# Performance work log

Hardware: AMD Instinct MI355X
Metric: run time of the kernel (lower is better)

The kernel has to match this reference:

```python
import jax, jax.numpy as jnp
import numpy as np

B, S, D = 2, 2048, 1024
N_HEADS = 16
HEAD_DIM = D // N_HEADS  # 64, even for RoPE
THETA = 10000.0


def rope_tables(seq, head_dim, dtype=jnp.float32):
    half = head_dim // 2
    freqs = 1.0 / (THETA ** (jnp.arange(half, dtype=jnp.float32) / half))
    angles = jnp.arange(seq, dtype=jnp.float32)[:, None] * freqs[None, :]  # [S, half]
    return jnp.cos(angles).astype(dtype), jnp.sin(angles).astype(dtype)


def apply_rope_interleaved(x, cos, sin):
    # x: [b, h, s, d]; even/odd interleaving
    x_even = x[..., 0::2]
    x_odd = x[..., 1::2]
    r_even = x_even * cos - x_odd * sin
    r_odd = x_even * sin + x_odd * cos
    # interleave back: stack on last axis then reshape
    out = jnp.stack([r_even, r_odd], axis=-1).reshape(x.shape)
    return out


def setup_inputs() -> dict:
    key = jax.random.key(0)
    ks = jax.random.split(key, 6)
    scale = 1.0 / np.sqrt(D)
    return {
        "x": jax.random.normal(ks[0], (B, S, D), dtype=jnp.float32),
        "Wq": jax.random.normal(ks[1], (D, D), dtype=jnp.float32) * scale,
        "Wk": jax.random.normal(ks[2], (D, D), dtype=jnp.float32) * scale,
        "Wv": jax.random.normal(ks[3], (D, D), dtype=jnp.float32) * scale,
        "Wo": jax.random.normal(ks[4], (D, D), dtype=jnp.float32) * scale,
        "bo": jnp.zeros((D,), dtype=jnp.float32),
    }


def reference(x, Wq, Wk, Wv, Wo, bo):
    b, s, _ = x.shape
    # QKV projections (no bias), split heads -> [b, h, s, hd]
    def proj(W):
        return jnp.einsum('bsd,de->bse', x, W).reshape(b, s, N_HEADS, HEAD_DIM).transpose(0, 2, 1, 3)
    q, k, v = proj(Wq), proj(Wk), proj(Wv)

    cos, sin = rope_tables(s, HEAD_DIM, x.dtype)  # [s, hd//2]
    q = apply_rope_interleaved(q, cos, sin)
    k = apply_rope_interleaved(k, cos, sin)

    scale = 1.0 / jnp.sqrt(jnp.asarray(HEAD_DIM, dtype=x.dtype))
    scores = jnp.einsum('bhqd,bhkd->bhqk', q, k) * scale  # [b, h, s, s]
    causal = jnp.tril(jnp.ones((s, s), dtype=bool))
    scores = jnp.where(causal[None, None], scores, jnp.asarray(-jnp.inf, dtype=scores.dtype))
    attn = jax.nn.softmax(scores, axis=-1)
    ctx = jnp.einsum('bhqk,bhkd->bhqd', attn, v)  # [b, h, s, hd]
    ctx = ctx.transpose(0, 2, 1, 3).reshape(b, s, N_HEADS * HEAD_DIM)
    return jnp.einsum('bsd,de->bse', ctx, Wo) + bo
```

## Files before the change

### kernel.cpp

```cpp
#include <hip/hip_runtime.h>
#include <hip/hip_bf16.h>
#include <math.h>

constexpr int Bb   = 2;
constexpr int S    = 2048;
constexpr int D    = 1024;
constexpr int H    = 16;
constexpr int Dh   = 64;
constexpr int HALF = 32;
constexpr int M    = Bb * S;
constexpr int K    = 1024;
constexpr int N    = 1024;

typedef __attribute__((ext_vector_type(8))) short short8;
typedef __attribute__((ext_vector_type(4))) float f32x4;

__device__ __forceinline__ unsigned short f2bf(float f) {
    unsigned int u = __float_as_uint(f);
    unsigned int r = (u + 0x7fffu + ((u >> 16) & 1u)) >> 16;
    return (unsigned short)r;
}

__device__ __forceinline__ void gl_lds16(const unsigned short* g, unsigned short* lds_base) {
    __builtin_amdgcn_global_load_lds(
        (const __attribute__((address_space(1))) unsigned int*)g,
        (__attribute__((address_space(3))) unsigned int*)lds_base, 16, 0, 0);
}

__global__ void rope_table_kernel(float* __restrict__ cosT, float* __restrict__ sinT) {
    int idx = blockIdx.x * blockDim.x + threadIdx.x;
    if (idx >= S * HALF) return;
    int s = idx / HALF;
    int i = idx % HALF;
    double freq = exp(-(double)i * (log(10000.0) / (double)HALF));
    double ang  = (double)s * freq;
    cosT[idx] = (float)cos(ang);
    sinT[idx] = (float)sin(ang);
}

__global__ __launch_bounds__(256) void convx_kernel(const float* __restrict__ x,
                                                    unsigned short* __restrict__ xb) {
    size_t i = (size_t)blockIdx.x * 256 + threadIdx.x;
    float4 v = *(const float4*)(x + i * 4);
    ushort4 pk;
    pk.x = f2bf(v.x); pk.y = f2bf(v.y); pk.z = f2bf(v.z); pk.w = f2bf(v.w);
    *(ushort4*)(xb + i * 4) = pk;
}

__global__ __launch_bounds__(256) void wt_kernel(
    const float* W0, const float* W1, const float* W2, const float* W3,
    unsigned short* T0, unsigned short* T1, unsigned short* T2, unsigned short* T3)
{
    __shared__ float tile[64][65];
    int z = blockIdx.z;
    const float* W = (z == 0) ? W0 : (z == 1) ? W1 : (z == 2) ? W2 : W3;
    unsigned short* T = (z == 0) ? T0 : (z == 1) ? T1 : (z == 2) ? T2 : T3;

    const int bk = blockIdx.y * 64;
    const int bn = blockIdx.x * 64;
    const int tid = threadIdx.x;
    const int lr = tid >> 4;
    const int lc = (tid & 15) * 4;

    #pragma unroll
    for (int i = 0; i < 4; ++i) {
        int r = lr + i * 16;
        float4 v = *(const float4*)(W + (size_t)(bk + r) * N + bn + lc);
        tile[r][lc + 0] = v.x; tile[r][lc + 1] = v.y;
        tile[r][lc + 2] = v.z; tile[r][lc + 3] = v.w;
    }
    __syncthreads();
    #pragma unroll
    for (int i = 0; i < 4; ++i) {
        int nr = lr + i * 16;
        ushort4 pk;
        pk.x = f2bf(tile[lc + 0][nr]);
        pk.y = f2bf(tile[lc + 1][nr]);
        pk.z = f2bf(tile[lc + 2][nr]);
        pk.w = f2bf(tile[lc + 3][nr]);
        *(ushort4*)(T + (size_t)(bn + nr) * K + bk + lc) = pk;
    }
}

__global__ __launch_bounds__(256) void mfma_gemm_kernel(
    const unsigned short* __restrict__ A,
    const unsigned short* BTa, const unsigned short* BTb, const unsigned short* BTc,
    void* outa, void* outb, void* outc,
    const float* __restrict__ bias,
    const float* __restrict__ cosT, const float* __restrict__ sinT,
    int fused)
{
    __shared__ __align__(16) unsigned short As[128 * 32];
    __shared__ __align__(16) unsigned short Bs[128 * 32];

    const int z = blockIdx.z;
    const unsigned short* BT = (z == 0) ? BTa : (z == 1) ? BTb : BTc;
    void* outp = (z == 0) ? outa : (z == 1) ? outb : outc;
    const int mode = fused ? ((z == 2) ? 2 : 1) : 0;

    const int tid  = threadIdx.x;
    const int wave = tid >> 6;
    const int lane = tid & 63;
    const int col  = lane & 15;
    const int quad = lane >> 4;
    const int wy   = wave >> 1;
    const int wx   = wave & 1;

    const int mbase = blockIdx.y * 128;
    const int nbase = blockIdx.x * 128;

    const int srow   = lane >> 2;
    const int schunk = lane & 3;

    f32x4 acc[4][4];
    #pragma unroll
    for (int mi = 0; mi < 4; ++mi)
        #pragma unroll
        for (int ni = 0; ni < 4; ++ni) acc[mi][ni] = (f32x4)0.f;

    for (int k0 = 0; k0 < K; k0 += 32) {
        __syncthreads();
        #pragma unroll
        for (int L = 0; L < 2; ++L) {
            int wrow = L * 64 + wave * 16;
            int tr   = wrow + srow;
            int gc   = (schunk + tr) & 3;
            gl_lds16(A  + (size_t)(mbase + tr) * K + k0 + gc * 8, &As[wrow * 32]);
            gl_lds16(BT + (size_t)(nbase + tr) * K + k0 + gc * 8, &Bs[wrow * 32]);
        }
        __syncthreads();

        short8 af[4], bf[4];
        #pragma unroll
        for (int mi = 0; mi < 4; ++mi) {
            int r = wy * 64 + mi * 16 + col;
            af[mi] = *(const short8*)&As[r * 32 + ((quad - r) & 3) * 8];
        }
        #pragma unroll
        for (int ni = 0; ni < 4; ++ni) {
            int r = wx * 64 + ni * 16 + col;
            bf[ni] = *(const short8*)&Bs[r * 32 + ((quad - r) & 3) * 8];
        }
        #pragma unroll
        for (int mi = 0; mi < 4; ++mi)
            #pragma unroll
            for (int ni = 0; ni < 4; ++ni)
                acc[mi][ni] = __builtin_amdgcn_mfma_f32_16x16x32_bf16(af[mi], bf[ni], acc[mi][ni], 0, 0, 0);
    }

    if (mode == 0) {
        float* o = (float*)outp;
        #pragma unroll
        for (int ni = 0; ni < 4; ++ni) {
            int n_g = nbase + wx * 64 + ni * 16 + col;
            float bv = bias[n_g];
            #pragma unroll
            for (int mi = 0; mi < 4; ++mi)
                #pragma unroll
                for (int reg = 0; reg < 4; ++reg) {
                    int m_g = mbase + wy * 64 + mi * 16 + quad * 4 + reg;
                    o[(size_t)m_g * N + n_g] = acc[mi][ni][reg] + bv;
                }
        }
    } else if (mode == 1) {
        unsigned short* o = (unsigned short*)outp;
        #pragma unroll
        for (int ni = 0; ni < 4; ++ni) {
            int n_g = nbase + wx * 64 + ni * 16 + col;
            int h = n_g >> 6, dh0 = n_g & 63, p = dh0 >> 1;
            bool even = !(dh0 & 1);
            #pragma unroll
            for (int mi = 0; mi < 4; ++mi)
                #pragma unroll
                for (int reg = 0; reg < 4; ++reg) {
                    int m_g = mbase + wy * 64 + mi * 16 + quad * 4 + reg;
                    int b = m_g >> 11, s = m_g & 2047;
                    float v = acc[mi][ni][reg];
                    float part = __shfl_xor(v, 1, 64);
                    float c = cosT[s * HALF + p], sn = sinT[s * HALF + p];
                    float r = even ? (v * c - part * sn) : (v * c + part * sn);
                    o[((size_t)(b * H + h) * S + s) * Dh + dh0] = f2bf(r);
                }
        }
    } else {
        unsigned short* o = (unsigned short*)outp;
        #pragma unroll
        for (int ni = 0; ni < 4; ++ni) {
            int n_g = nbase + wx * 64 + ni * 16 + col;
            int h = n_g >> 6, dh0 = n_g & 63;
            #pragma unroll
            for (int mi = 0; mi < 4; ++mi) {
                int m0g = mbase + wy * 64 + mi * 16 + quad * 4;
                int b = m0g >> 11, s = m0g & 2047;
                ushort4 pk;
                pk.x = f2bf(acc[mi][ni][0]);
                pk.y = f2bf(acc[mi][ni][1]);
                pk.z = f2bf(acc[mi][ni][2]);
                pk.w = f2bf(acc[mi][ni][3]);
                *(ushort4*)&o[((size_t)(b * H + h) * Dh + dh0) * S + s] = pk;
            }
        }
    }
}

__global__ __launch_bounds__(256) void attn_mfma_kernel(
    const unsigned short* __restrict__ q, const unsigned short* __restrict__ k,
    const unsigned short* __restrict__ vt, unsigned short* __restrict__ ctx)
{
    __shared__ __align__(16) short Ks[64 * 64];
    __shared__ __align__(16) short Vs[64 * 64];
    __shared__ __align__(16) short Ps[4][16 * 72];

    const int tid  = threadIdx.x;
    const int wave = tid >> 6;
    const int lane = tid & 63;
    const int col  = lane & 15;
    const int quad = lane >> 4;
    const int l8   = lane >> 3, cp = lane & 7;

    const int bh = blockIdx.y;
    const unsigned short* qb = q  + (size_t)bh * S * Dh;
    const unsigned short* kb = k  + (size_t)bh * S * Dh;
    const unsigned short* vb = vt + (size_t)bh * Dh * S;
    const int b = bh >> 4, h = bh & 15;

    for (int phase = 0; phase < 2; ++phase) {
        const int qt  = phase ? (31 - (int)blockIdx.x) : (int)blockIdx.x;
        const int wr0 = qt * 64 + wave * 16;

        short8 qfrag[2];
        #pragma unroll
        for (int ks = 0; ks < 2; ++ks)
            qfrag[ks] = *(const short8*)(qb + (size_t)(wr0 + col) * Dh + ks * 32 + quad * 8);

        f32x4 O[4];
        float lacc[4];
        #pragma unroll
        for (int nt = 0; nt < 4; ++nt) O[nt] = (f32x4)0.f;
        #pragma unroll
        for (int r = 0; r < 4; ++r) lacc[r] = 0.f;

        short8 kr[2], vr[2];
        #pragma unroll
        for (int c = 0; c < 2; ++c) {
            int row = wave * 16 + c * 8 + l8;
            int sc  = (cp + row) & 7;
            kr[c] = *(const short8*)(kb + (size_t)row * Dh + sc * 8);
            vr[c] = *(const short8*)(vb + (size_t)row * S + sc * 8);
        }

        for (int t = 0; t <= qt; ++t) {
            __syncthreads();
            #pragma unroll
            for (int c = 0; c < 2; ++c) {
                int row = wave * 16 + c * 8 + l8;
                *(short8*)&Ks[row * 64 + cp * 8] = kr[c];
                *(short8*)&Vs[row * 64 + cp * 8] = vr[c];
            }
            __syncthreads();
            if (t < qt) {
                #pragma unroll
                for (int c = 0; c < 2; ++c) {
                    int row = wave * 16 + c * 8 + l8;
                    int sc  = (cp + row) & 7;
                    kr[c] = *(const short8*)(kb + (size_t)((t + 1) * 64 + row) * Dh + sc * 8);
                    vr[c] = *(const short8*)(vb + (size_t)row * S + (t + 1) * 64 + sc * 8);
                }
            }

            f32x4 sacc[4];
            #pragma unroll
            for (int nt = 0; nt < 4; ++nt) sacc[nt] = (f32x4)0.f;
            #pragma unroll
            for (int ks = 0; ks < 2; ++ks) {
                #pragma unroll
                for (int nt = 0; nt < 4; ++nt) {
                    int key = nt * 16 + col;
                    short8 kf = *(const short8*)&Ks[key * 64 + (((ks * 4 + quad) - key) & 7) * 8];
                    sacc[nt] = __builtin_amdgcn_mfma_f32_16x16x32_bf16(qfrag[ks], kf, sacc[nt], 0, 0, 0);
                }
            }

            float pb[4][4];
            #pragma unroll
            for (int nt = 0; nt < 4; ++nt) {
                int key_l = nt * 16 + col;
                #pragma unroll
                for (int reg = 0; reg < 4; ++reg) {
                    float e = __expf(fmaf(sacc[nt][reg], 0.125f, -8.0f));
                    if (t == qt && key_l > wave * 16 + quad * 4 + reg) e = 0.f;
                    pb[nt][reg] = e;
                }
            }
            #pragma unroll
            for (int reg = 0; reg < 4; ++reg)
                lacc[reg] += (pb[0][reg] + pb[1][reg]) + (pb[2][reg] + pb[3][reg]);

            #pragma unroll
            for (int nt = 0; nt < 4; ++nt)
                #pragma unroll
                for (int reg = 0; reg < 4; ++reg)
                    Ps[wave][(quad * 4 + reg) * 72 + nt * 16 + col] = (short)f2bf(pb[nt][reg]);

            #pragma unroll
            for (int ks = 0; ks < 2; ++ks) {
                short8 pf = *(const short8*)&Ps[wave][col * 72 + ks * 32 + quad * 8];
                #pragma unroll
                for (int nt = 0; nt < 4; ++nt) {
                    int dh = nt * 16 + col;
                    short8 vf = *(const short8*)&Vs[dh * 64 + (((ks * 4 + quad) - dh) & 7) * 8];
                    O[nt] = __builtin_amdgcn_mfma_f32_16x16x32_bf16(pf, vf, O[nt], 0, 0, 0);
                }
            }
        }

        #pragma unroll
        for (int reg = 0; reg < 4; ++reg) {
            float s = lacc[reg];
            #pragma unroll
            for (int off = 1; off <= 8; off <<= 1)
                s += __shfl_xor(s, off, 64);
            lacc[reg] = s;
        }

        #pragma unroll
        for (int reg = 0; reg < 4; ++reg) {
            float inv = 1.0f / lacc[reg];
            int rg = wr0 + quad * 4 + reg;
            unsigned short* dst = ctx + ((size_t)b * S + rg) * 1024 + h * 64 + col;
            #pragma unroll
            for (int nt = 0; nt < 4; ++nt)
                dst[nt * 16] = f2bf(O[nt][reg] * inv);
        }
    }
}

extern "C" void kernel_launch(void* const* d_in, const int* in_sizes, int n_in,
                              void* d_out, int out_size, void* d_ws, size_t ws_size,
                              hipStream_t stream) {
    const float* x  = (const float*)d_in[0];
    const float* Wq = (const float*)d_in[1];
    const float* Wk = (const float*)d_in[2];
    const float* Wv = (const float*)d_in[3];
    const float* Wo = (const float*)d_in[4];
    const float* bo = (const float*)d_in[5];
    float* out = (float*)d_out;

    const size_t MK  = (size_t)M * K;
    const size_t NK  = (size_t)N * K;
    const size_t QKV = (size_t)Bb * H * S * Dh;

    unsigned short* xb   = (unsigned short*)d_ws;
    unsigned short* WqT  = xb  + MK;
    unsigned short* WkT  = WqT + NK;
    unsigned short* WvT  = WkT + NK;
    unsigned short* WoT  = WvT + NK;
    unsigned short* qbuf = WoT + NK;
    unsigned short* kbuf = qbuf + QKV;
    unsigned short* vtb  = kbuf + QKV;
    unsigned short* ctxb = vtb  + QKV;
    float* cosT = (float*)(ctxb + QKV);
    float* sinT = cosT + (size_t)S * HALF;

    rope_table_kernel<<<(S * HALF + 255) / 256, 256, 0, stream>>>(cosT, sinT);
    convx_kernel<<<(int)(MK / 4 / 256), 256, 0, stream>>>(x, xb);
    wt_kernel<<<dim3(16, 16, 4), 256, 0, stream>>>(Wq, Wk, Wv, Wo, WqT, WkT, WvT, WoT);

    mfma_gemm_kernel<<<dim3(8, 32, 3), 256, 0, stream>>>(
        xb, WqT, WkT, WvT, qbuf, kbuf, vtb, nullptr, cosT, sinT, 1);

    attn_mfma_kernel<<<dim3(16, Bb * H), 256, 0, stream>>>(qbuf, kbuf, vtb, ctxb);

    mfma_gemm_kernel<<<dim3(8, 32, 1), 256, 0, stream>>>(
        ctxb, WoT, nullptr, nullptr, out, nullptr, nullptr, bo, cosT, sinT, 0);
}
```

Measured before the change: 211.1 us.

## Share A tile across fused Q/K/V projections with narrower N tiles

After: 222.8 us. +5.5%, slower.

```diff
diff --git a/kernel.cpp b/kernel.cpp
--- a/kernel.cpp
+++ b/kernel.cpp
@@ -82,21 +82,19 @@
     }
 }
 
+template<int NZ, int MODEQ>
 __global__ __launch_bounds__(256) void mfma_gemm_kernel(
     const unsigned short* __restrict__ A,
-    const unsigned short* BTa, const unsigned short* BTb, const unsigned short* BTc,
-    void* outa, void* outb, void* outc,
+    const unsigned short* BT0, const unsigned short* BT1, const unsigned short* BT2,
+    void* out0, void* out1, void* out2,
     const float* __restrict__ bias,
-    const float* __restrict__ cosT, const float* __restrict__ sinT,
-    int fused)
+    const float* __restrict__ cosT, const float* __restrict__ sinT)
 {
     __shared__ __align__(16) unsigned short As[128 * 32];
-    __shared__ __align__(16) unsigned short Bs[128 * 32];
-
-    const int z = blockIdx.z;
-    const unsigned short* BT = (z == 0) ? BTa : (z == 1) ? BTb : BTc;
-    void* outp = (z == 0) ? outa : (z == 1) ? outb : outc;
-    const int mode = fused ? ((z == 2) ? 2 : 1) : 0;
+    __shared__ __align__(16) unsigned short Bs[NZ][64 * 32];
+
+    const unsigned short* BT[3] = {BT0, BT1, BT2};
+    void* outs[3] = {out0, out1, out2};
 
     const int tid  = threadIdx.x;
     const int wave = tid >> 6;
@@ -107,16 +105,18 @@
     const int wx   = wave & 1;
 
     const int mbase = blockIdx.y * 128;
-    const int nbase = blockIdx.x * 128;
+    const int nbase = blockIdx.x * 64;
 
     const int srow   = lane >> 2;
     const int schunk = lane & 3;
 
-    f32x4 acc[4][4];
+    f32x4 acc[NZ][4][2];
     #pragma unroll
-    for (int mi = 0; mi < 4; ++mi)
-        #pragma unroll
-        for (int ni = 0; ni < 4; ++ni) acc[mi][ni] = (f32x4)0.f;
+    for (int z = 0; z < NZ; ++z)
+        #pragma unroll
+        for (int mi = 0; mi < 4; ++mi)
+            #pragma unroll
+            for (int ni = 0; ni < 2; ++ni) acc[z][mi][ni] = (f32x4)0.f;
 
     for (int k0 = 0; k0 < K; k0 += 32) {
         __syncthreads();
@@ -124,80 +124,95 @@
         for (int L = 0; L < 2; ++L) {
             int wrow = L * 64 + wave * 16;
             int tr   = wrow + srow;
-            int gc   = (schunk + tr) & 3;
-            gl_lds16(A  + (size_t)(mbase + tr) * K + k0 + gc * 8, &As[wrow * 32]);
-            gl_lds16(BT + (size_t)(nbase + tr) * K + k0 + gc * 8, &Bs[wrow * 32]);
+            int gc   = (schunk + (tr >> 1)) & 3;
+            gl_lds16(A + (size_t)(mbase + tr) * K + k0 + gc * 8, &As[wrow * 32]);
+        }
+        {
+            int wrow = wave * 16;
+            int tr   = wrow + srow;
+            int gc   = (schunk + (tr >> 1)) & 3;
+            #pragma unroll
+            for (int z = 0; z < NZ; ++z)
+                gl_lds16(BT[z] + (size_t)(nbase + tr) * K + k0 + gc * 8, &Bs[z][wrow * 32]);
         }
         __syncthreads();
 
-        short8 af[4], bf[4];
+        short8 af[4], bf[NZ][2];
         #pragma unroll
         for (int mi = 0; mi < 4; ++mi) {
             int r = wy * 64 + mi * 16 + col;
-            af[mi] = *(const short8*)&As[r * 32 + ((quad - r) & 3) * 8];
-        }
-        #pragma unroll
-        for (int ni = 0; ni < 4; ++ni) {
-            int r = wx * 64 + ni * 16 + col;
-            bf[ni] = *(const short8*)&Bs[r * 32 + ((quad - r) & 3) * 8];
-        }
-        #pragma unroll
-        for (int mi = 0; mi < 4; ++mi)
-            #pragma unroll
-            for (int ni = 0; ni < 4; ++ni)
-                acc[mi][ni] = __builtin_amdgcn_mfma_f32_16x16x32_bf16(af[mi], bf[ni], acc[mi][ni], 0, 0, 0);
-    }
-
-    if (mode == 0) {
-        float* o = (float*)outp;
-        #pragma unroll
-        for (int ni = 0; ni < 4; ++ni) {
-            int n_g = nbase + wx * 64 + ni * 16 + col;
-            float bv = bias[n_g];
+            af[mi] = *(const short8*)&As[r * 32 + ((quad - (r >> 1)) & 3) * 8];
+        }
+        #pragma unroll
+        for (int z = 0; z < NZ; ++z)
+            #pragma unroll
+            for (int ni = 0; ni < 2; ++ni) {
+                int r = wx * 32 + ni * 16 + col;
+                bf[z][ni] = *(const short8*)&Bs[z][r * 32 + ((quad - (r >> 1)) & 3) * 8];
+            }
+        #pragma unroll
+        for (int z = 0; z < NZ; ++z)
             #pragma unroll
             for (int mi = 0; mi < 4; ++mi)
                 #pragma unroll
-                for (int reg = 0; reg < 4; ++reg) {
-                    int m_g = mbase + wy * 64 + mi * 16 + quad * 4 + reg;
-                    o[(size_t)m_g * N + n_g] = acc[mi][ni][reg] + bv;
-                }
-        }
-    } else if (mode == 1) {
-        unsigned short* o = (unsigned short*)outp;
-        #pragma unroll
-        for (int ni = 0; ni < 4; ++ni) {
-            int n_g = nbase + wx * 64 + ni * 16 + col;
-            int h = n_g >> 6, dh0 = n_g & 63, p = dh0 >> 1;
-            bool even = !(dh0 & 1);
-            #pragma unroll
-            for (int mi = 0; mi < 4; ++mi)
-                #pragma unroll
-                for (int reg = 0; reg < 4; ++reg) {
-                    int m_g = mbase + wy * 64 + mi * 16 + quad * 4 + reg;
-                    int b = m_g >> 11, s = m_g & 2047;
-                    float v = acc[mi][ni][reg];
-                    float part = __shfl_xor(v, 1, 64);
-                    float c = cosT[s * HALF + p], sn = sinT[s * HALF + p];
-                    float r = even ? (v * c - part * sn) : (v * c + part * sn);
-                    o[((size_t)(b * H + h) * S + s) * Dh + dh0] = f2bf(r);
-                }
-        }
-    } else {
-        unsigned short* o = (unsigned short*)outp;
-        #pragma unroll
-        for (int ni = 0; ni < 4; ++ni) {
-            int n_g = nbase + wx * 64 + ni * 16 + col;
-            int h = n_g >> 6, dh0 = n_g & 63;
-            #pragma unroll
-            for (int mi = 0; mi < 4; ++mi) {
-                int m0g = mbase + wy * 64 + mi * 16 + quad * 4;
-                int b = m0g >> 11, s = m0g & 2047;
-                ushort4 pk;
-                pk.x = f2bf(acc[mi][ni][0]);
-                pk.y = f2bf(acc[mi][ni][1]);
-                pk.z = f2bf(acc[mi][ni][2]);
-                pk.w = f2bf(acc[mi][ni][3]);
-                *(ushort4*)&o[((size_t)(b * H + h) * Dh + dh0) * S + s] = pk;
+                for (int ni = 0; ni < 2; ++ni)
+                    acc[z][mi][ni] = __builtin_amdgcn_mfma_f32_16x16x32_bf16(
+                        af[mi], bf[z][ni], acc[z][mi][ni], 0, 0, 0);
+    }
+
+    #pragma unroll
+    for (int z = 0; z < NZ; ++z) {
+        if (MODEQ == 0) {
+            float* o = (float*)outs[z];
+            #pragma unroll
+            for (int ni = 0; ni < 2; ++ni) {
+                int n_g = nbase + wx * 32 + ni * 16 + col;
+                float bv = bias[n_g];
+                #pragma unroll
+                for (int mi = 0; mi < 4; ++mi)
+                    #pragma unroll
+                    for (int reg = 0; reg < 4; ++reg) {
+                        int m_g = mbase + wy * 64 + mi * 16 + quad * 4 + reg;
+                        o[(size_t)m_g * N + n_g] = acc[z][mi][ni][reg] + bv;
+                    }
+            }
+        } else if (z < 2) {
+            unsigned short* o = (unsigned short*)outs[z];
+            #pragma unroll
+            for (int ni = 0; ni < 2; ++ni) {
+                int n_g = nbase + wx * 32 + ni * 16 + col;
+                int h = n_g >> 6, dh0 = n_g & 63, p = dh0 >> 1;
+                bool even = !(dh0 & 1);
+                #pragma unroll
+                for (int mi = 0; mi < 4; ++mi)
+                    #pragma unroll
+                    for (int reg = 0; reg < 4; ++reg) {
+                        int m_g = mbase + wy * 64 + mi * 16 + quad * 4 + reg;
+                        int b = m_g >> 11, s = m_g & 2047;
+                        float v = acc[z][mi][ni][reg];
+                        float part = __shfl_xor(v, 1, 64);
+                        float c = cosT[s * HALF + p], sn = sinT[s * HALF + p];
+                        float r = even ? (v * c - part * sn) : (v * c + part * sn);
+                        o[((size_t)(b * H + h) * S + s) * Dh + dh0] = f2bf(r);
+                    }
+            }
+        } else {
+            unsigned short* o = (unsigned short*)outs[z];
+            #pragma unroll
+            for (int ni = 0; ni < 2; ++ni) {
+                int n_g = nbase + wx * 32 + ni * 16 + col;
+                int h = n_g >> 6, dh0 = n_g & 63;
+                #pragma unroll
+                for (int mi = 0; mi < 4; ++mi) {
+                    int m0g = mbase + wy * 64 + mi * 16 + quad * 4;
+                    int b = m0g >> 11, s = m0g & 2047;
+                    ushort4 pk;
+                    pk.x = f2bf(acc[z][mi][ni][0]);
+                    pk.y = f2bf(acc[z][mi][ni][1]);
+                    pk.z = f2bf(acc[z][mi][ni][2]);
+                    pk.w = f2bf(acc[z][mi][ni][3]);
+                    *(ushort4*)&o[((size_t)(b * H + h) * Dh + dh0) * S + s] = pk;
+                }
             }
         }
     }
@@ -366,11 +381,11 @@
     convx_kernel<<<(int)(MK / 4 / 256), 256, 0, stream>>>(x, xb);
     wt_kernel<<<dim3(16, 16, 4), 256, 0, stream>>>(Wq, Wk, Wv, Wo, WqT, WkT, WvT, WoT);
 
-    mfma_gemm_kernel<<<dim3(8, 32, 3), 256, 0, stream>>>(
-        xb, WqT, WkT, WvT, qbuf, kbuf, vtb, nullptr, cosT, sinT, 1);
+    mfma_gemm_kernel<3, 1><<<dim3(16, 32), 256, 0, stream>>>(
+        xb, WqT, WkT, WvT, qbuf, kbuf, vtb, nullptr, cosT, sinT);
 
     attn_mfma_kernel<<<dim3(16, Bb * H), 256, 0, stream>>>(qbuf, kbuf, vtb, ctxb);
 
-    mfma_gemm_kernel<<<dim3(8, 32, 1), 256, 0, stream>>>(
-        ctxb, WoT, nullptr, nullptr, out, nullptr, nullptr, bo, cosT, sinT, 0);
-}
+    mfma_gemm_kernel<1, 0><<<dim3(16, 32), 256, 0, stream>>>(
+        ctxb, WoT, WoT, WoT, out, out, out, bo, cosT, sinT);
+}
```

## Double-buffer LDS with async global-to-LDS loads in GEMM and attention

Applied to the files above, without the earlier changes.

New measurement: 216.1 us. +2.4%, slower.

```diff
diff --git a/kernel.cpp b/kernel.cpp
--- a/kernel.cpp
+++ b/kernel.cpp
@@ -82,21 +82,16 @@
     }
 }
 
+template<int MODE>
 __global__ __launch_bounds__(256) void mfma_gemm_kernel(
     const unsigned short* __restrict__ A,
-    const unsigned short* BTa, const unsigned short* BTb, const unsigned short* BTc,
-    void* outa, void* outb, void* outc,
-    const float* __restrict__ bias,
-    const float* __restrict__ cosT, const float* __restrict__ sinT,
-    int fused)
+    const unsigned short* __restrict__ BT,
+    unsigned short* outQ, unsigned short* outK, unsigned short* outV,
+    float* outO, const float* __restrict__ bias,
+    const float* __restrict__ cosT, const float* __restrict__ sinT)
 {
-    __shared__ __align__(16) unsigned short As[128 * 32];
-    __shared__ __align__(16) unsigned short Bs[128 * 32];
-
-    const int z = blockIdx.z;
-    const unsigned short* BT = (z == 0) ? BTa : (z == 1) ? BTb : BTc;
-    void* outp = (z == 0) ? outa : (z == 1) ? outb : outc;
-    const int mode = fused ? ((z == 2) ? 2 : 1) : 0;
+    __shared__ __align__(16) unsigned short As[2][128 * 32];
+    __shared__ __align__(16) unsigned short Bs[2][128 * 32];
 
     const int tid  = threadIdx.x;
     const int wave = tid >> 6;
@@ -118,28 +113,34 @@
         #pragma unroll
         for (int ni = 0; ni < 4; ++ni) acc[mi][ni] = (f32x4)0.f;
 
-    for (int k0 = 0; k0 < K; k0 += 32) {
-        __syncthreads();
+    auto stage = [&](int buf, int k0) {
         #pragma unroll
         for (int L = 0; L < 2; ++L) {
             int wrow = L * 64 + wave * 16;
             int tr   = wrow + srow;
-            int gc   = (schunk + tr) & 3;
-            gl_lds16(A  + (size_t)(mbase + tr) * K + k0 + gc * 8, &As[wrow * 32]);
-            gl_lds16(BT + (size_t)(nbase + tr) * K + k0 + gc * 8, &Bs[wrow * 32]);
-        }
+            int gc   = (schunk + (tr >> 1)) & 3;
+            gl_lds16(A  + (size_t)(mbase + tr) * K + k0 + gc * 8, &As[buf][wrow * 32]);
+            gl_lds16(BT + (size_t)(nbase + tr) * K + k0 + gc * 8, &Bs[buf][wrow * 32]);
+        }
+    };
+
+    stage(0, 0);
+    for (int kk = 0; kk < K / 32; ++kk) {
         __syncthreads();
-
+        if (kk + 1 < K / 32) stage((kk + 1) & 1, (kk + 1) * 32);
+
+        const unsigned short* Ac = As[kk & 1];
+        const unsigned short* Bc = Bs[kk & 1];
         short8 af[4], bf[4];
         #pragma unroll
         for (int mi = 0; mi < 4; ++mi) {
             int r = wy * 64 + mi * 16 + col;
-            af[mi] = *(const short8*)&As[r * 32 + ((quad - r) & 3) * 8];
+            af[mi] = *(const short8*)&Ac[r * 32 + ((quad - (r >> 1)) & 3) * 8];
         }
         #pragma unroll
         for (int ni = 0; ni < 4; ++ni) {
             int r = wx * 64 + ni * 16 + col;
-            bf[ni] = *(const short8*)&Bs[r * 32 + ((quad - r) & 3) * 8];
+            bf[ni] = *(const short8*)&Bc[r * 32 + ((quad - (r >> 1)) & 3) * 8];
         }
         #pragma unroll
         for (int mi = 0; mi < 4; ++mi)
@@ -148,8 +149,7 @@
                 acc[mi][ni] = __builtin_amdgcn_mfma_f32_16x16x32_bf16(af[mi], bf[ni], acc[mi][ni], 0, 0, 0);
     }
 
-    if (mode == 0) {
-        float* o = (float*)outp;
+    if (MODE == 0) {
         #pragma unroll
         for (int ni = 0; ni < 4; ++ni) {
             int n_g = nbase + wx * 64 + ni * 16 + col;
@@ -159,45 +159,48 @@
                 #pragma unroll
                 for (int reg = 0; reg < 4; ++reg) {
                     int m_g = mbase + wy * 64 + mi * 16 + quad * 4 + reg;
-                    o[(size_t)m_g * N + n_g] = acc[mi][ni][reg] + bv;
-                }
-        }
-    } else if (mode == 1) {
-        unsigned short* o = (unsigned short*)outp;
-        #pragma unroll
-        for (int ni = 0; ni < 4; ++ni) {
-            int n_g = nbase + wx * 64 + ni * 16 + col;
-            int h = n_g >> 6, dh0 = n_g & 63, p = dh0 >> 1;
-            bool even = !(dh0 & 1);
-            #pragma unroll
-            for (int mi = 0; mi < 4; ++mi)
-                #pragma unroll
-                for (int reg = 0; reg < 4; ++reg) {
-                    int m_g = mbase + wy * 64 + mi * 16 + quad * 4 + reg;
-                    int b = m_g >> 11, s = m_g & 2047;
-                    float v = acc[mi][ni][reg];
-                    float part = __shfl_xor(v, 1, 64);
-                    float c = cosT[s * HALF + p], sn = sinT[s * HALF + p];
-                    float r = even ? (v * c - part * sn) : (v * c + part * sn);
-                    o[((size_t)(b * H + h) * S + s) * Dh + dh0] = f2bf(r);
+                    outO[(size_t)m_g * N + n_g] = acc[mi][ni][reg] + bv;
                 }
         }
     } else {
-        unsigned short* o = (unsigned short*)outp;
-        #pragma unroll
-        for (int ni = 0; ni < 4; ++ni) {
-            int n_g = nbase + wx * 64 + ni * 16 + col;
-            int h = n_g >> 6, dh0 = n_g & 63;
-            #pragma unroll
-            for (int mi = 0; mi < 4; ++mi) {
-                int m0g = mbase + wy * 64 + mi * 16 + quad * 4;
-                int b = m0g >> 11, s = m0g & 2047;
-                ushort4 pk;
-                pk.x = f2bf(acc[mi][ni][0]);
-                pk.y = f2bf(acc[mi][ni][1]);
-                pk.z = f2bf(acc[mi][ni][2]);
-                pk.w = f2bf(acc[mi][ni][3]);
-                *(ushort4*)&o[((size_t)(b * H + h) * Dh + dh0) * S + s] = pk;
+        const int z = nbase >> 10;
+        if (z < 2) {
+            unsigned short* o = z ? outK : outQ;
+            #pragma unroll
+            for (int ni = 0; ni < 4; ++ni) {
+                int nl = (nbase & 1023) + wx * 64 + ni * 16 + col;
+                int h = nl >> 6, dh0 = nl & 63, p = dh0 >> 1;
+                bool even = !(dh0 & 1);
+                #pragma unroll
+                for (int mi = 0; mi < 4; ++mi)
+                    #pragma unroll
+                    for (int reg = 0; reg < 4; ++reg) {
+                        int m_g = mbase + wy * 64 + mi * 16 + quad * 4 + reg;
+                        int b = m_g >> 11, s = m_g & 2047;
+                        float v = acc[mi][ni][reg];
+                        float part = __shfl_xor(v, 1, 64);
+                        float c = cosT[s * HALF + p], sn = sinT[s * HALF + p];
+                        float r = even ? (v * c - part * sn) : (v * c + part * sn);
+                        o[((size_t)(b * H + h) * S + s) * Dh + dh0] = f2bf(r);
+                    }
+            }
+        } else {
+            unsigned short* o = outV;
+            #pragma unroll
+            for (int ni = 0; ni < 4; ++ni) {
+                int nl = (nbase & 1023) + wx * 64 + ni * 16 + col;
+                int h = nl >> 6, dh0 = nl & 63;
+                #pragma unroll
+                for (int mi = 0; mi < 4; ++mi) {
+                    int m0g = mbase + wy * 64 + mi * 16 + quad * 4;
+                    int b = m0g >> 11, s = m0g & 2047;
+                    ushort4 pk;
+                    pk.x = f2bf(acc[mi][ni][0]);
+                    pk.y = f2bf(acc[mi][ni][1]);
+                    pk.z = f2bf(acc[mi][ni][2]);
+                    pk.w = f2bf(acc[mi][ni][3]);
+                    *(ushort4*)&o[((size_t)(b * H + h) * Dh + dh0) * S + s] = pk;
+                }
             }
         }
     }
@@ -207,8 +210,8 @@
     const unsigned short* __restrict__ q, const unsigned short* __restrict__ k,
     const unsigned short* __restrict__ vt, unsigned short* __restrict__ ctx)
 {
-    __shared__ __align__(16) short Ks[64 * 64];
-    __shared__ __align__(16) short Vs[64 * 64];
+    __shared__ __align__(16) short Ks[2][64 * 64];
+    __shared__ __align__(16) short Vs[2][64 * 64];
     __shared__ __align__(16) short Ps[4][16 * 72];
 
     const int tid  = threadIdx.x;
@@ -224,10 +227,25 @@
     const unsigned short* vb = vt + (size_t)bh * Dh * S;
     const int b = bh >> 4, h = bh & 15;
 
+    auto stage = [&](int buf, int t) {
+        #pragma unroll
+        for (int c = 0; c < 2; ++c) {
+            int row = wave * 16 + c * 8 + l8;
+            int sc  = (cp + row) & 7;
+            gl_lds16(kb + (size_t)(t * 64 + row) * Dh + sc * 8,
+                     (unsigned short*)&Ks[buf][(wave * 16 + c * 8) * 64]);
+            gl_lds16(vb + (size_t)row * S + t * 64 + sc * 8,
+                     (unsigned short*)&Vs[buf][(wave * 16 + c * 8) * 64]);
+        }
+    };
+
     for (int phase = 0; phase < 2; ++phase) {
         const int qt  = phase ? (31 - (int)blockIdx.x) : (int)blockIdx.x;
         const int wr0 = qt * 64 + wave * 16;
 
+        __syncthreads();
+        stage(0, 0);
+
         short8 qfrag[2];
         #pragma unroll
         for (int ks = 0; ks < 2; ++ks)
@@ -240,33 +258,12 @@
         #pragma unroll
         for (int r = 0; r < 4; ++r) lacc[r] = 0.f;
 
-        short8 kr[2], vr[2];
-        #pragma unroll
-        for (int c = 0; c < 2; ++c) {
-            int row = wave * 16 + c * 8 + l8;
-            int sc  = (cp + row) & 7;
-            kr[c] = *(const short8*)(kb + (size_t)row * Dh + sc * 8);
-            vr[c] = *(const short8*)(vb + (size_t)row * S + sc * 8);
-        }
-
         for (int t = 0; t <= qt; ++t) {
             __syncthreads();
-            #pragma unroll
-            for (int c = 0; c < 2; ++c) {
-                int row = wave * 16 + c * 8 + l8;
-                *(short8*)&Ks[row * 64 + cp * 8] = kr[c];
-                *(short8*)&Vs[row * 64 + cp * 8] = vr[c];
-            }
-            __syncthreads();
-            if (t < qt) {
-                #pragma unroll
-                for (int c = 0; c < 2; ++c) {
-                    int row = wave * 16 + c * 8 + l8;
-                    int sc  = (cp + row) & 7;
-                    kr[c] = *(const short8*)(kb + (size_t)((t + 1) * 64 + row) * Dh + sc * 8);
-                    vr[c] = *(const short8*)(vb + (size_t)row * S + (t + 1) * 64 + sc * 8);
-                }
-            }
+            if (t < qt) stage((t + 1) & 1, t + 1);
+
+            const short* Kc = Ks[t & 1];
+            const short* Vc = Vs[t & 1];
 
             f32x4 sacc[4];
             #pragma unroll
@@ -276,7 +273,7 @@
                 #pragma unroll
                 for (int nt = 0; nt < 4; ++nt) {
                     int key = nt * 16 + col;
-                    short8 kf = *(const short8*)&Ks[key * 64 + (((ks * 4 + quad) - key) & 7) * 8];
+                    short8 kf = *(const short8*)&Kc[key * 64 + (((ks * 4 + quad) - key) & 7) * 8];
                     sacc[nt] = __builtin_amdgcn_mfma_f32_16x16x32_bf16(qfrag[ks], kf, sacc[nt], 0, 0, 0);
                 }
             }
@@ -308,7 +305,7 @@
                 #pragma unroll
                 for (int nt = 0; nt < 4; ++nt) {
                     int dh = nt * 16 + col;
-                    short8 vf = *(const short8*)&Vs[dh * 64 + (((ks * 4 + quad) - dh) & 7) * 8];
+                    short8 vf = *(const short8*)&Vc[dh * 64 + (((ks * 4 + quad) - dh) & 7) * 8];
                     O[nt] = __builtin_amdgcn_mfma_f32_16x16x32_bf16(pf, vf, O[nt], 0, 0, 0);
                 }
             }
@@ -366,11 +363,11 @@
     convx_kernel<<<(int)(MK / 4 / 256), 256, 0, stream>>>(x, xb);
     wt_kernel<<<dim3(16, 16, 4), 256, 0, stream>>>(Wq, Wk, Wv, Wo, WqT, WkT, WvT, WoT);
 
-    mfma_gemm_kernel<<<dim3(8, 32, 3), 256, 0, stream>>>(
-        xb, WqT, WkT, WvT, qbuf, kbuf, vtb, nullptr, cosT, sinT, 1);
+    mfma_gemm_kernel<1><<<dim3(24, 32), 256, 0, stream>>>(
+        xb, WqT, qbuf, kbuf, vtb, nullptr, nullptr, cosT, sinT);
 
     attn_mfma_kernel<<<dim3(16, Bb * H), 256, 0, stream>>>(qbuf, kbuf, vtb, ctxb);
 
-    mfma_gemm_kernel<<<dim3(8, 32, 1), 256, 0, stream>>>(
-        ctxb, WoT, nullptr, nullptr, out, nullptr, nullptr, bo, cosT, sinT, 0);
-}
+    mfma_gemm_kernel<0><<<dim3(8, 32), 256, 0, stream>>>(
+        ctxb, WoT, nullptr, nullptr, nullptr, out, bo, cosT, sinT);
+}
```
